# Performance work log

Measured on AMD Instinct MI355X. Metric: run time of the kernel, lower is better.

Reference implementation:

```python
import jax, jax.numpy as jnp
import numpy as np

B, L, V, N = 2, 2048, 32000, 1024  # batch, seq, vocab, n_embd (ambient dim = N+1)


def _sanitize(x):
    return jnp.nan_to_num(x, nan=0.0, posinf=1e4, neginf=-1e4)


def _safe_acosh(x):
    # safe_acosh_v2: Taylor expansion near x=1 to avoid gradient explosion.
    xm1 = jnp.maximum(x - 1.0, 0.0)
    near = xm1 < 1e-3
    taylor = jnp.sqrt(2.0 * jnp.maximum(xm1, 1e-12)) * (1.0 - xm1 / 12.0)
    exact = jnp.arccosh(jnp.maximum(x, 1.0 + 1e-7))
    return jnp.where(near, taylor, exact)


def setup_inputs() -> dict:
    key = jax.random.key(0)
    k1, k2 = jax.random.split(key)
    # Build valid Lorentz points on H^n: x0 = sqrt(1 + ||x_spatial||^2)
    sp = 0.5 * jax.random.normal(k1, (B, L, N), dtype=jnp.float32)
    t = jnp.sqrt(1.0 + jnp.sum(sp * sp, axis=-1, keepdims=True))
    hidden_states = jnp.concatenate([t, sp], axis=-1)  # [B, L, N+1]
    weight = 0.01 * jax.random.normal(k2, (V, N), dtype=jnp.float32)  # tangent vectors
    logit_scale = jnp.asarray(1.0 / np.sqrt(N), dtype=jnp.float32)  # init_logit_scale/sqrt(n_embd)
    return {"hidden_states": hidden_states, "weight": weight, "logit_scale": logit_scale}


def reference(hidden_states, weight, logit_scale):
    h = _sanitize(hidden_states)
    # exp_map_zero of zero-padded tangent vectors [V, N] -> hyperboloid points [V, N+1]
    # exp_o(v) = cosh(||v||) * o + sinh(||v||)/||v|| * v, with o = (1, 0, ..., 0)
    norm = jnp.linalg.norm(weight, axis=-1)  # [V]
    r = jnp.where(norm > 1e-7, jnp.sinh(norm) / jnp.maximum(norm, 1e-7), 1.0)
    w_time = jnp.cosh(norm)          # [V]
    w_space = r[:, None] * weight    # [V, N]
    # Lorentz distance: d = acosh(-<h, w>_L), -<h,w>_L = h0*w0 - h_sp . w_sp
    # Expressed as a GEMM over the vocab instead of a [B,L,V,N+1] broadcast.
    x = h[..., :1] * w_time[None, None, :] - jnp.einsum('bln,vn->blv', h[..., 1:], w_space)
    d = _safe_acosh(x)  # [B, L, V]
    tau = jnp.clip(logit_scale, 0.01, 2.5)
    logits = -tau * d * d
    return _sanitize(logits)
```

## Files before the change

### kernel.cpp

```cpp
#include <hip/hip_runtime.h>
#include <hip/hip_bf16.h>
#include <hip/hip_fp8.h>
#include <math.h>

#define M_TOT 4096
#define K_TOT 1024
#define V_TOT 32000

typedef int int4v __attribute__((ext_vector_type(4)));
typedef int int8v __attribute__((ext_vector_type(8)));
typedef float f32x4 __attribute__((ext_vector_type(4)));

__device__ __forceinline__ void gload_lds16(const void* g, void* l) {
  __builtin_amdgcn_global_load_lds(
      (const __attribute__((address_space(1))) void*)g,
      (__attribute__((address_space(3))) void*)l, 16, 0, 0);
}

__device__ __forceinline__ float sani(float v) {
  return (v != v) ? 0.0f : fminf(fmaxf(v, -1e4f), 1e4f);
}

__device__ __forceinline__ int pk4_fp8(float a, float b, float c, float d) {
#if __has_builtin(__builtin_amdgcn_cvt_pk_fp8_f32)
  int p = __builtin_amdgcn_cvt_pk_fp8_f32(a, b, 0, false);
  p = __builtin_amdgcn_cvt_pk_fp8_f32(c, d, p, true);
  return p;
#else
  union { unsigned char b4[4]; int i; } u;
  u.b4[0] = __hip_fp8_e4m3(a).__x;
  u.b4[1] = __hip_fp8_e4m3(b).__x;
  u.b4[2] = __hip_fp8_e4m3(c).__x;
  u.b4[3] = __hip_fp8_e4m3(d).__x;
  return u.i;
#endif
}

__global__ void prep_h(const float* __restrict__ h, unsigned char* __restrict__ h8,
                       float* __restrict__ h0) {
  int m = blockIdx.x;
  int t = threadIdx.x;
  const float* row = h + (long)m * (K_TOT + 1);
  if (t == 0) h0[m] = sani(row[0]);
  float4 x = *(const float4*)(row + 1 + t * 4);
  ((int*)(h8 + (long)m * K_TOT))[t] =
      pk4_fp8(sani(x.x), sani(x.y), sani(x.z), sani(x.w));
}

__global__ void prep_w(const float* __restrict__ w, unsigned char* __restrict__ w8,
                       float* __restrict__ wtime) {
  __shared__ float red[4];
  __shared__ float r_sh;
  int v = blockIdx.x;
  int t = threadIdx.x;
  const float* row = w + (long)v * K_TOT;
  float4 x = *(const float4*)(row + t * 4);
  float s = x.x * x.x + x.y * x.y + x.z * x.z + x.w * x.w;
#pragma unroll
  for (int off = 32; off > 0; off >>= 1) s += __shfl_down(s, off);
  int lane = t & 63, wv = t >> 6;
  if (lane == 0) red[wv] = s;
  __syncthreads();
  if (t == 0) {
    float tot = red[0] + red[1] + red[2] + red[3];
    float norm = sqrtf(tot);
    float r = (norm > 1e-7f) ? (sinhf(norm) / fmaxf(norm, 1e-7f)) : 1.0f;
    r_sh = r;
    wtime[v] = coshf(norm);
  }
  __syncthreads();
  float sc = 16.0f * r_sh;
  ((int*)(w8 + (long)v * K_TOT))[t] =
      pk4_fp8(sc * x.x, sc * x.y, sc * x.z, sc * x.w);
}

#define BAR __builtin_amdgcn_s_barrier()
#define LGKM0 asm volatile("s_waitcnt lgkmcnt(0)" ::: "memory")
#define VM8 asm volatile("s_waitcnt vmcnt(8)" ::: "memory")

__global__ __launch_bounds__(512, 2) void gemm_geo(
    const unsigned char* __restrict__ h8, const unsigned char* __restrict__ w8,
    const float* __restrict__ h0, const float* __restrict__ wtime,
    const float* __restrict__ ls, float* __restrict__ out) {
  __shared__ __align__(16) char smem[131072];

  const int t = threadIdx.x;
  const int wave = t >> 6, lane = t & 63;
  const int fr = lane & 15, fq = lane >> 4;
  const int wm = wave >> 2, wn = wave & 3;

  const int bid = blockIdx.x;
  const int swz = (bid & 7) * 250 + (bid >> 3);
  const int tile_v = swz >> 4;
  const int tile_m = swz & 15;
  const int row0 = tile_m * 256;
  const int col0 = tile_v * 256;

  const int xorv = fr & 7;
  const int c0 = ((2 * fq) ^ xorv) * 16;
  const int c1 = ((2 * fq + 1) ^ xorv) * 16;
  const int a_base = (wm * 128 + fr) * 128;
  const int b_base = 32768 + (wn * 64 + fr) * 128;

  auto RDF = [&](int off) -> int8v {
    int4v lo = *(const int4v*)(smem + off + c0);
    int4v hi = *(const int4v*)(smem + off + c1);
    return (int8v){lo[0], lo[1], lo[2], lo[3], hi[0], hi[1], hi[2], hi[3]};
  };

  const int cc = (t & 7) ^ ((t >> 3) & 7);
  const unsigned char* pA = h8 + ((long)row0 + (t >> 3)) * K_TOT + cc * 16;
  const unsigned char* pB = w8 + ((long)col0 + (t >> 3)) * K_TOT + cc * 16;
  const int dst_w = wave * 1024;

  auto STAGE = [&](int kt, int bufo) {
#pragma unroll
    for (int hh = 0; hh < 4; ++hh) {
      gload_lds16(pA + (long)hh * 65536 + kt * 128,
                  smem + bufo + hh * 8192 + dst_w);
      gload_lds16(pB + (long)hh * 65536 + kt * 128,
                  smem + bufo + 32768 + hh * 8192 + dst_w);
    }
  };

  f32x4 acc[8][4];
#pragma unroll
  for (int i = 0; i < 8; ++i)
#pragma unroll
    for (int j = 0; j < 4; ++j) acc[i][j] = (f32x4)(0.0f);

  STAGE(0, 0);
  STAGE(1, 65536);
  VM8;
  BAR;

#pragma unroll 1
  for (int kt = 0; kt < 8; ++kt) {
    const int cbo = (kt & 1) << 16;
    const int skt = (kt + 2 < 8) ? kt + 2 : 7;

    int8v bv[4], av[4];
#pragma unroll
    for (int iv = 0; iv < 4; ++iv) bv[iv] = RDF(cbo + b_base + iv * 2048);
#pragma unroll
    for (int im = 0; im < 4; ++im) av[im] = RDF(cbo + a_base + im * 2048);

    __builtin_amdgcn_s_setprio(1);
#pragma unroll
    for (int im = 0; im < 4; ++im)
#pragma unroll
      for (int iv = 0; iv < 4; ++iv)
        acc[im][iv] = __builtin_amdgcn_mfma_scale_f32_16x16x128_f8f6f4(
            bv[iv], av[im], acc[im][iv], 0, 0, 0, 0x7B7B7B7B, 0, 0x7F7F7F7F);
    __builtin_amdgcn_s_setprio(0);

    int8v av2[4];
#pragma unroll
    for (int im = 0; im < 4; ++im)
      av2[im] = RDF(cbo + a_base + (4 + im) * 2048);
    LGKM0;
    __builtin_amdgcn_sched_barrier(0);
    BAR;

    STAGE(skt, cbo);

    __builtin_amdgcn_s_setprio(1);
#pragma unroll
    for (int im = 0; im < 4; ++im)
#pragma unroll
      for (int iv = 0; iv < 4; ++iv)
        acc[4 + im][iv] = __builtin_amdgcn_mfma_scale_f32_16x16x128_f8f6f4(
            bv[iv], av2[im], acc[4 + im][iv], 0, 0, 0, 0x7B7B7B7B, 0,
            0x7F7F7F7F);
    __builtin_amdgcn_s_setprio(0);

    VM8;
    BAR;
  }

  const float ntau = -fminf(fmaxf(ls[0], 0.01f), 2.5f);
  const float LN2 = 0.69314718055994531f;
  f32x4 wt4[4];
#pragma unroll
  for (int iv = 0; iv < 4; ++iv)
    wt4[iv] = *(const f32x4*)&wtime[col0 + wn * 64 + iv * 16 + fq * 4];
#pragma unroll
  for (int im = 0; im < 8; ++im) {
    const float hh = h0[row0 + wm * 128 + im * 16 + fr];
    float* orow =
        out + (long)(row0 + wm * 128 + im * 16 + fr) * V_TOT + col0 + wn * 64;
#pragma unroll
    for (int iv = 0; iv < 4; ++iv) {
      f32x4 r;
#pragma unroll
      for (int j = 0; j < 4; ++j) {
        float x = fmaf(hh, wt4[iv][j], -acc[im][iv][j]);
        float xm1 = fmaxf(x - 1.0f, 0.0f);
        float arg = fmaxf(fmaf(x, x, -1.0f), 0.0f);
        float lg2 = __builtin_amdgcn_logf(x + __builtin_amdgcn_sqrtf(arg));
        float dex = LN2 * lg2;
        float d2_exact = dex * dex;
        float ts = fmaf(xm1, -1.0f / 12.0f, 1.0f);
        float d2_tay = 2.0f * xm1 * ts * ts;
        float d2 = (xm1 < 1e-3f) ? d2_tay : d2_exact;
        r[j] = ntau * d2;
      }
      *(f32x4*)(orow + iv * 16 + fq * 4) = r;
    }
  }
}

extern "C" void kernel_launch(void* const* d_in, const int* in_sizes, int n_in,
                              void* d_out, int out_size, void* d_ws, size_t ws_size,
                              hipStream_t stream) {
  const float* h = (const float*)d_in[0];
  const float* w = (const float*)d_in[1];
  const float* ls = (const float*)d_in[2];
  float* out = (float*)d_out;

  char* ws = (char*)d_ws;
  unsigned char* w8 = (unsigned char*)ws;
  unsigned char* h8 = (unsigned char*)(ws + 32768000);
  float* wtime = (float*)(ws + 32768000 + 4194304);
  float* h0 = (float*)(ws + 32768000 + 4194304 + 128000);

  prep_h<<<M_TOT, 256, 0, stream>>>(h, h8, h0);
  prep_w<<<V_TOT, 256, 0, stream>>>(w, w8, wtime);
  gemm_geo<<<2000, 512, 0, stream>>>(h8, w8, h0, wtime, ls, out);
}
```

Before: 289.9 us.

## Make GEMM persistent over M tiles and overlap epilogue stores with next tile's MMA

Measured after the change: 334.2 us. +15.3%, slower.

```diff
diff --git a/kernel.cpp b/kernel.cpp
--- a/kernel.cpp
+++ b/kernel.cpp
@@ -75,14 +75,81 @@
 }
 
 #define BAR __builtin_amdgcn_s_barrier()
-#define LGKM0 asm volatile("s_waitcnt lgkmcnt(0)" ::: "memory")
-#define VM8 asm volatile("s_waitcnt vmcnt(8)" ::: "memory")
+#define VMC(N) asm volatile("s_waitcnt vmcnt(" #N ")" ::: "memory")
+
+#define STORE_CHUNK(KT, ACCO, H0O)                                            \
+  {                                                                           \
+    const int imo = (KT) >> 1;                                                \
+    const int iv0 = ((KT) & 1) * 2;                                           \
+    float* obase_ = orow_old + imo * (16L * V_TOT);                           \
+    _Pragma("unroll") for (int dv = 0; dv < 2; ++dv) {                        \
+      const int iv = iv0 + dv;                                                \
+      f32x4 rr;                                                               \
+      _Pragma("unroll") for (int j = 0; j < 4; ++j) {                         \
+        float x = fmaf(H0O[imo], wt4[iv][j], -ACCO[imo][iv][j]);              \
+        float xm1 = fmaxf(x - 1.0f, 0.0f);                                    \
+        float arg = fmaxf(fmaf(x, x, -1.0f), 0.0f);                           \
+        float lg2 = __builtin_amdgcn_logf(x + __builtin_amdgcn_sqrtf(arg));   \
+        float dex = 0.69314718055994531f * lg2;                               \
+        float d2e = dex * dex;                                                \
+        float ts = fmaf(xm1, -1.0f / 12.0f, 1.0f);                            \
+        float d2t = 2.0f * xm1 * ts * ts;                                     \
+        rr[j] = ntau * ((xm1 < 1e-3f) ? d2t : d2e);                           \
+      }                                                                       \
+      *(f32x4*)(obase_ + iv * 16 + fq * 4) = rr;                              \
+      ACCO[imo][iv] = (f32x4)(0.0f);                                          \
+    }                                                                         \
+  }
+
+#define KITER(KT, DO_PRE, H0N, ACC, DO_ST, ACCO, H0O, VMN)                    \
+  {                                                                           \
+    if (DO_PRE) {                                                             \
+      _Pragma("unroll") for (int im = 0; im < 4; ++im)                        \
+          H0N[im] = h0p[im * 16];                                             \
+    }                                                                         \
+    int gs = g + (KT) + 2;                                                    \
+    if (gs > 127) gs = 127;                                                   \
+    STAGE(gs, sbv);                                                           \
+    if (DO_ST) { STORE_CHUNK(KT, ACCO, H0O); }                                \
+    const int CBO = cbv * 49152;                                              \
+    int8v bv0 = RDF(CBO + b_rd);                                              \
+    int8v bv1 = RDF(CBO + b_rd + 2048);                                       \
+    int8v bv2 = RDF(CBO + b_rd + 4096);                                       \
+    int8v bv3 = RDF(CBO + b_rd + 6144);                                       \
+    __builtin_amdgcn_s_setprio(1);                                            \
+    _Pragma("unroll") for (int im = 0; im < 4; ++im) {                        \
+      int8v av = RDF(CBO + a_rd + im * 2048);                                 \
+      ACC[im][0] = __builtin_amdgcn_mfma_scale_f32_16x16x128_f8f6f4(          \
+          bv0, av, ACC[im][0], 0, 0, 0, 0x7B7B7B7B, 0, 0x7F7F7F7F);           \
+      ACC[im][1] = __builtin_amdgcn_mfma_scale_f32_16x16x128_f8f6f4(          \
+          bv1, av, ACC[im][1], 0, 0, 0, 0x7B7B7B7B, 0, 0x7F7F7F7F);           \
+      ACC[im][2] = __builtin_amdgcn_mfma_scale_f32_16x16x128_f8f6f4(          \
+          bv2, av, ACC[im][2], 0, 0, 0, 0x7B7B7B7B, 0, 0x7F7F7F7F);           \
+      ACC[im][3] = __builtin_amdgcn_mfma_scale_f32_16x16x128_f8f6f4(          \
+          bv3, av, ACC[im][3], 0, 0, 0, 0x7B7B7B7B, 0, 0x7F7F7F7F);           \
+    }                                                                         \
+    __builtin_amdgcn_s_setprio(0);                                            \
+    VMC(VMN);                                                                 \
+    BAR;                                                                      \
+    cbv = (cbv == 2) ? 0 : cbv + 1;                                           \
+    sbv = (sbv == 2) ? 0 : sbv + 1;                                           \
+  }
+
+#define KT8(DO_PRE, H0N, ACC, DO_ST, ACCO, H0O, VM0, VMR)                     \
+  KITER(0, DO_PRE, H0N, ACC, DO_ST, ACCO, H0O, VM0)                           \
+  KITER(1, 0, H0N, ACC, DO_ST, ACCO, H0O, VMR)                                \
+  KITER(2, 0, H0N, ACC, DO_ST, ACCO, H0O, VMR)                                \
+  KITER(3, 0, H0N, ACC, DO_ST, ACCO, H0O, VMR)                                \
+  KITER(4, 0, H0N, ACC, DO_ST, ACCO, H0O, VMR)                                \
+  KITER(5, 0, H0N, ACC, DO_ST, ACCO, H0O, VMR)                                \
+  KITER(6, 0, H0N, ACC, DO_ST, ACCO, H0O, VMR)                                \
+  KITER(7, 0, H0N, ACC, DO_ST, ACCO, H0O, VMR)
 
 __global__ __launch_bounds__(512, 2) void gemm_geo(
     const unsigned char* __restrict__ h8, const unsigned char* __restrict__ w8,
     const float* __restrict__ h0, const float* __restrict__ wtime,
     const float* __restrict__ ls, float* __restrict__ out) {
-  __shared__ __align__(16) char smem[131072];
+  __shared__ __align__(16) char smem[147456];
 
   const int t = threadIdx.x;
   const int wave = t >> 6, lane = t & 63;
@@ -90,17 +157,16 @@
   const int wm = wave >> 2, wn = wave & 3;
 
   const int bid = blockIdx.x;
-  const int swz = (bid & 7) * 250 + (bid >> 3);
-  const int tile_v = swz >> 4;
-  const int tile_m = swz & 15;
-  const int row0 = tile_m * 256;
-  const int col0 = tile_v * 256;
+  const int p = bid >> 1;
+  const int q = bid & 1;
+  const int col0 = p * 256;
+  const int mrow_base = q * 2048;
 
   const int xorv = fr & 7;
   const int c0 = ((2 * fq) ^ xorv) * 16;
   const int c1 = ((2 * fq + 1) ^ xorv) * 16;
-  const int a_base = (wm * 128 + fr) * 128;
-  const int b_base = 32768 + (wn * 64 + fr) * 128;
+  const int a_rd = (wm * 64 + fr) * 128;
+  const int b_rd = 16384 + (wn * 64 + fr) * 128;
 
   auto RDF = [&](int off) -> int8v {
     int4v lo = *(const int4v*)(smem + off + c0);
@@ -109,103 +175,101 @@
   };
 
   const int cc = (t & 7) ^ ((t >> 3) & 7);
-  const unsigned char* pA = h8 + ((long)row0 + (t >> 3)) * K_TOT + cc * 16;
+  const unsigned char* pA = h8 + ((long)mrow_base + (t >> 3)) * K_TOT + cc * 16;
   const unsigned char* pB = w8 + ((long)col0 + (t >> 3)) * K_TOT + cc * 16;
   const int dst_w = wave * 1024;
 
-  auto STAGE = [&](int kt, int bufo) {
-#pragma unroll
-    for (int hh = 0; hh < 4; ++hh) {
-      gload_lds16(pA + (long)hh * 65536 + kt * 128,
-                  smem + bufo + hh * 8192 + dst_w);
-      gload_lds16(pB + (long)hh * 65536 + kt * 128,
-                  smem + bufo + 32768 + hh * 8192 + dst_w);
-    }
+  auto STAGE = [&](int gg, int sb) {
+    const int itv = gg >> 3, ktv = gg & 7;
+    const unsigned char* a = pA + (long)itv * (128L * K_TOT) + ktv * 128;
+    const unsigned char* b = pB + ktv * 128;
+    const int bo = sb * 49152;
+#pragma unroll
+    for (int hh = 0; hh < 2; ++hh)
+      gload_lds16(a + (long)hh * (64L * K_TOT), smem + bo + hh * 8192 + dst_w);
+#pragma unroll
+    for (int hh = 0; hh < 4; ++hh)
+      gload_lds16(b + (long)hh * (64L * K_TOT),
+                  smem + bo + 16384 + hh * 8192 + dst_w);
   };
 
-  f32x4 acc[8][4];
-#pragma unroll
-  for (int i = 0; i < 8; ++i)
-#pragma unroll
-    for (int j = 0; j < 4; ++j) acc[i][j] = (f32x4)(0.0f);
-
-  STAGE(0, 0);
-  STAGE(1, 65536);
-  VM8;
-  BAR;
-
-#pragma unroll 1
-  for (int kt = 0; kt < 8; ++kt) {
-    const int cbo = (kt & 1) << 16;
-    const int skt = (kt + 2 < 8) ? kt + 2 : 7;
-
-    int8v bv[4], av[4];
-#pragma unroll
-    for (int iv = 0; iv < 4; ++iv) bv[iv] = RDF(cbo + b_base + iv * 2048);
-#pragma unroll
-    for (int im = 0; im < 4; ++im) av[im] = RDF(cbo + a_base + im * 2048);
-
-    __builtin_amdgcn_s_setprio(1);
-#pragma unroll
-    for (int im = 0; im < 4; ++im)
-#pragma unroll
-      for (int iv = 0; iv < 4; ++iv)
-        acc[im][iv] = __builtin_amdgcn_mfma_scale_f32_16x16x128_f8f6f4(
-            bv[iv], av[im], acc[im][iv], 0, 0, 0, 0x7B7B7B7B, 0, 0x7F7F7F7F);
-    __builtin_amdgcn_s_setprio(0);
-
-    int8v av2[4];
-#pragma unroll
-    for (int im = 0; im < 4; ++im)
-      av2[im] = RDF(cbo + a_base + (4 + im) * 2048);
-    LGKM0;
-    __builtin_amdgcn_sched_barrier(0);
-    BAR;
-
-    STAGE(skt, cbo);
-
-    __builtin_amdgcn_s_setprio(1);
-#pragma unroll
-    for (int im = 0; im < 4; ++im)
-#pragma unroll
-      for (int iv = 0; iv < 4; ++iv)
-        acc[4 + im][iv] = __builtin_amdgcn_mfma_scale_f32_16x16x128_f8f6f4(
-            bv[iv], av2[im], acc[4 + im][iv], 0, 0, 0, 0x7B7B7B7B, 0,
-            0x7F7F7F7F);
-    __builtin_amdgcn_s_setprio(0);
-
-    VM8;
-    BAR;
-  }
-
   const float ntau = -fminf(fmaxf(ls[0], 0.01f), 2.5f);
-  const float LN2 = 0.69314718055994531f;
   f32x4 wt4[4];
 #pragma unroll
   for (int iv = 0; iv < 4; ++iv)
     wt4[iv] = *(const f32x4*)&wtime[col0 + wn * 64 + iv * 16 + fq * 4];
-#pragma unroll
-  for (int im = 0; im < 8; ++im) {
-    const float hh = h0[row0 + wm * 128 + im * 16 + fr];
-    float* orow =
-        out + (long)(row0 + wm * 128 + im * 16 + fr) * V_TOT + col0 + wn * 64;
-#pragma unroll
-    for (int iv = 0; iv < 4; ++iv) {
-      f32x4 r;
-#pragma unroll
-      for (int j = 0; j < 4; ++j) {
-        float x = fmaf(hh, wt4[iv][j], -acc[im][iv][j]);
-        float xm1 = fmaxf(x - 1.0f, 0.0f);
-        float arg = fmaxf(fmaf(x, x, -1.0f), 0.0f);
-        float lg2 = __builtin_amdgcn_logf(x + __builtin_amdgcn_sqrtf(arg));
-        float dex = LN2 * lg2;
-        float d2_exact = dex * dex;
-        float ts = fmaf(xm1, -1.0f / 12.0f, 1.0f);
-        float d2_tay = 2.0f * xm1 * ts * ts;
-        float d2 = (xm1 < 1e-3f) ? d2_tay : d2_exact;
-        r[j] = ntau * d2;
+
+  f32x4 accA[4][4], accB[4][4];
+#pragma unroll
+  for (int i = 0; i < 4; ++i)
+#pragma unroll
+    for (int j = 0; j < 4; ++j) {
+      accA[i][j] = (f32x4)(0.0f);
+      accB[i][j] = (f32x4)(0.0f);
+    }
+  float h0A[4], h0B[4];
+
+  const float* h0p = h0 + mrow_base + wm * 64 + fr;
+#pragma unroll
+  for (int im = 0; im < 4; ++im) h0A[im] = h0p[im * 16];
+  STAGE(0, 0);
+  STAGE(1, 1);
+  VMC(0);
+  BAR;
+
+  int cbv = 0, sbv = 2;
+  int g = 0;
+  float* orow_old;
+
+  KT8(0, h0A, accA, 0, accB, h0B, 6, 6)
+  g = 8;
+
+  h0p = h0 + mrow_base + 128 + wm * 64 + fr;
+  orow_old = out + ((long)(mrow_base + wm * 64 + fr)) * V_TOT + col0 + wn * 64;
+  KT8(1, h0B, accB, 1, accA, h0A, 12, 10)
+  g = 16;
+
+#pragma unroll 1
+  for (int ith = 1; ith <= 7; ++ith) {
+    const int ite = 2 * ith;
+    h0p = h0 + mrow_base + ite * 128 + wm * 64 + fr;
+    orow_old = out +
+               ((long)(mrow_base + (ite - 1) * 128 + wm * 64 + fr)) * V_TOT +
+               col0 + wn * 64;
+    KT8(1, h0A, accA, 1, accB, h0B, 14, 10)
+    g += 8;
+
+    h0p = h0 + mrow_base + (ite + 1) * 128 + wm * 64 + fr;
+    orow_old = out + ((long)(mrow_base + ite * 128 + wm * 64 + fr)) * V_TOT +
+               col0 + wn * 64;
+    KT8(1, h0B, accB, 1, accA, h0A, 14, 10)
+    g += 8;
+  }
+
+  {
+    float* orow = out +
+                  ((long)(mrow_base + 15 * 128 + wm * 64 + fr)) * V_TOT +
+                  col0 + wn * 64;
+#pragma unroll
+    for (int im = 0; im < 4; ++im) {
+      float* obase = orow + im * (16L * V_TOT);
+#pragma unroll
+      for (int iv = 0; iv < 4; ++iv) {
+        f32x4 rr;
+#pragma unroll
+        for (int j = 0; j < 4; ++j) {
+          float x = fmaf(h0B[im], wt4[iv][j], -accB[im][iv][j]);
+          float xm1 = fmaxf(x - 1.0f, 0.0f);
+          float arg = fmaxf(fmaf(x, x, -1.0f), 0.0f);
+          float lg2 = __builtin_amdgcn_logf(x + __builtin_amdgcn_sqrtf(arg));
+          float dex = 0.69314718055994531f * lg2;
+          float d2e = dex * dex;
+          float ts = fmaf(xm1, -1.0f / 12.0f, 1.0f);
+          float d2t = 2.0f * xm1 * ts * ts;
+          rr[j] = ntau * ((xm1 < 1e-3f) ? d2t : d2e);
+        }
+        *(f32x4*)(obase + iv * 16 + fq * 4) = rr;
       }
-      *(f32x4*)(orow + iv * 16 + fq * 4) = r;
     }
   }
 }
@@ -226,5 +290,5 @@
 
   prep_h<<<M_TOT, 256, 0, stream>>>(h, h8, h0);
   prep_w<<<V_TOT, 256, 0, stream>>>(w, w8, wtime);
-  gemm_geo<<<2000, 512, 0, stream>>>(h8, w8, h0, wtime, ls, out);
-}
+  gemm_geo<<<250, 512, 0, stream>>>(h8, w8, h0, wtime, ls, out);
+}
```
